# Kernel optimization log

Measured on AMD Instinct MI355X. Metric: run time of the kernel, lower is better.

Reference implementation:

```python
import jax, jax.numpy as jnp
from jax import lax
import numpy as np

B, DIM, HEADS, L, K = 8, 128, 8, 4096, 3
INNER = DIM * HEADS
PAD = K // 2
EPS = 1e-5
SCALE = DIM ** -0.5


def setup_inputs() -> dict:
    key = jax.random.key(0)
    ks = jax.random.split(key, 32)

    def n(i, shape, s):
        return jax.random.normal(ks[i], shape, jnp.float32) * s

    inp = {"x": jax.random.normal(ks[0], (B, DIM, L), jnp.float32)}
    inp["ln1_g"] = jnp.ones((DIM,), jnp.float32)
    inp["ln1_b"] = jnp.zeros((DIM,), jnp.float32)
    for idx, p in enumerate(("q", "k", "v")):
        base = 1 + idx * 2
        inp[p + "_dw"] = n(base, (DIM, 1, K), 0.2)        # depthwise kernel
        inp[p + "_bn_g"] = jnp.ones((DIM,), jnp.float32)
        inp[p + "_bn_b"] = jnp.zeros((DIM,), jnp.float32)
        inp[p + "_bn_m"] = jnp.zeros((DIM,), jnp.float32)  # running mean
        inp[p + "_bn_v"] = jnp.ones((DIM,), jnp.float32)   # running var
        inp[p + "_pw"] = n(base + 1, (INNER, DIM), 0.05)   # 1x1 conv dim->inner
    inp["dwc_dw"] = n(8, (DIM,), 0.2)                      # kernel-1 depthwise = per-channel scale
    inp["dwc_bn_g"] = jnp.ones((DIM,), jnp.float32)
    inp["dwc_bn_b"] = jnp.zeros((DIM,), jnp.float32)
    inp["dwc_bn_m"] = jnp.zeros((DIM,), jnp.float32)
    inp["dwc_bn_v"] = jnp.ones((DIM,), jnp.float32)
    inp["dwc_pw"] = n(9, (DIM, DIM), 0.05)
    inp["out_w"] = n(10, (DIM, INNER), 0.05)
    inp["out_b"] = jnp.zeros((DIM,), jnp.float32)
    inp["ln2_g"] = jnp.ones((DIM,), jnp.float32)
    inp["ln2_b"] = jnp.zeros((DIM,), jnp.float32)
    inp["ff_w1"] = n(11, (4 * DIM, DIM), 0.05)
    inp["ff_b1"] = jnp.zeros((4 * DIM,), jnp.float32)
    inp["ff_w2"] = n(12, (DIM, 4 * DIM), 0.05)
    inp["ff_b2"] = jnp.zeros((DIM,), jnp.float32)
    return inp


def _layernorm(x, g, b):
    # channel-wise LN over axis=1 (unbiased=False variance)
    m = jnp.mean(x, axis=1, keepdims=True)
    v = jnp.var(x, axis=1, keepdims=True)
    return (x - m) / jnp.sqrt(v + EPS) * g[None, :, None] + b[None, :, None]


def _dw_block(x, dw, g, b, m, v, pw):
    # depthwise conv (k=K, same padding) -> eval-mode BN -> 1x1 conv
    y = lax.conv_general_dilated(x, dw, (1,), [(PAD, PAD)],
                                 feature_group_count=DIM,
                                 dimension_numbers=("NCH", "OIH", "NCH"))
    y = (y - m[None, :, None]) * (g / jnp.sqrt(v + EPS))[None, :, None] + b[None, :, None]
    return jnp.einsum("oi,bil->bol", pw, y)


def reference(x, ln1_g, ln1_b,
              q_dw, q_bn_g, q_bn_b, q_bn_m, q_bn_v, q_pw,
              k_dw, k_bn_g, k_bn_b, k_bn_m, k_bn_v, k_pw,
              v_dw, v_bn_g, v_bn_b, v_bn_m, v_bn_v, v_pw,
              dwc_dw, dwc_bn_g, dwc_bn_b, dwc_bn_m, dwc_bn_v, dwc_pw,
              out_w, out_b, ln2_g, ln2_b, ff_w1, ff_b1, ff_w2, ff_b2):
    # ---- attention block (PreNorm + residual) ----
    xn = _layernorm(x, ln1_g, ln1_b)
    q = _dw_block(xn, q_dw, q_bn_g, q_bn_b, q_bn_m, q_bn_v, q_pw)  # [B, INNER, L]
    k = _dw_block(xn, k_dw, k_bn_g, k_bn_b, k_bn_m, k_bn_v, k_pw)
    v = _dw_block(xn, v_dw, v_bn_g, v_bn_b, v_bn_m, v_bn_v, v_pw)

    def split(t):  # b (h d) x -> (b h) x d
        return t.reshape(B, HEADS, DIM, L).transpose(0, 1, 3, 2).reshape(B * HEADS, L, DIM)

    q, k, v = split(q), split(k), split(v)
    k_soft = jax.nn.softmax(k, axis=-1)                       # softmax over feature dim d
    kk = jnp.einsum("nxd,nxe->nde", q, k_soft) * SCALE        # [(bh), d, d]
    # DWConv gate on q (kernel-1 depthwise -> BN -> 1x1), channels = DIM
    g_ = q * dwc_dw[None, None, :]
    g_ = (g_ - dwc_bn_m) * (dwc_bn_g / jnp.sqrt(dwc_bn_v + EPS)) + dwc_bn_b
    g_ = jnp.einsum("od,nxd->nxo", dwc_pw, g_)
    gate = jax.nn.sigmoid(g_) * v
    out = jnp.einsum("nxd,nde->nxe", v, kk) + gate            # [(bh), L, d]
    out = out.reshape(B, HEADS, L, DIM).transpose(0, 1, 3, 2).reshape(B, INNER, L)
    attn = jnp.einsum("oi,bil->bol", out_w, out) + out_b[None, :, None]
    x = attn + x

    # ---- feed-forward block (PreNorm + residual) ----
    xn = _layernorm(x, ln2_g, ln2_b)
    h = jnp.einsum("oi,bil->bol", ff_w1, xn) + ff_b1[None, :, None]
    h = jax.nn.gelu(h, approximate=False)
    h = jnp.einsum("oi,bil->bol", ff_w2, h) + ff_b2[None, :, None]
    return h + x
```

## Files before the change

### kernel.cpp

```cpp
#include <hip/hip_runtime.h>
#include <hip/hip_bf16.h>
#include <math.h>

#define DI __device__ __forceinline__

namespace {

constexpr int L = 4096;
constexpr float EPS = 1e-5f;
constexpr float SCALEF = 0.08838834764831845f;

typedef unsigned short u16;
typedef unsigned int u32;
typedef unsigned char u8;
typedef __attribute__((ext_vector_type(8))) short bf16x8;
typedef __attribute__((ext_vector_type(4))) float f32x4;

DI float b2f(u16 h){ u32 u = ((u32)h) << 16; float f; __builtin_memcpy(&f, &u, 4); return f; }
DI u16 f2b(float f){ u32 u; __builtin_memcpy(&u, &f, 4); u32 r = u + 0x7fffu + ((u >> 16) & 1u); return (u16)(r >> 16); }
DI float sigmoidf(float x){ return 1.f / (1.f + __expf(-x)); }

DI uint2 pack_fp8x8(const float* v){
  u32 lo = __builtin_amdgcn_cvt_pk_fp8_f32(v[0], v[1], 0, false);
  lo = (u32)__builtin_amdgcn_cvt_pk_fp8_f32(v[2], v[3], lo, true);
  u32 hi = __builtin_amdgcn_cvt_pk_fp8_f32(v[4], v[5], 0, false);
  hi = (u32)__builtin_amdgcn_cvt_pk_fp8_f32(v[6], v[7], hi, true);
  return make_uint2(lo, hi);
}
DI u8 f2e(float v){ return (u8)__builtin_amdgcn_cvt_pk_fp8_f32(v, v, 0, false); }
DI float e2f(u8 c){ return __builtin_amdgcn_cvt_f32_fp8((int)c, 0); }

DI int boff(int o, int d8){ return ((o >> 4) << 11) + (d8 << 7) + (((o & 15) ^ d8) << 3); }
DI int toff(int dhi, int nl, int x8){ return (dhi << 11) + (x8 << 7) + (((nl ^ x8 ^ dhi) & 15) << 3); }
DI int foff(int g, int k8, int nn){ return (g << 11) + (k8 << 7) + (nn << 3); }
DI int faddr(int x, int e){ return ((x >> 4) << 11) + ((e >> 3) << 7) + ((x & 15) << 3) + (e & 7); }

DI void stage_a(const u16* __restrict__ g, int rs, u16* a_s, int tid){
  #pragma unroll
  for (int it = 0; it < 4; it++){
    int item = tid + 256 * it;
    int d8 = item & 15, l = item >> 4;
    *(uint4*)&a_s[l * 136 + d8 * 8] = *(const uint4*)&g[(size_t)l * rs + d8 * 8];
  }
}

__global__ __launch_bounds__(256) void ln_kernel(
    const float* __restrict__ x, const float* __restrict__ g,
    const float* __restrict__ bt, u16* __restrict__ o)
{
  const int tid = threadIdx.x;
  const int pos = blockIdx.x * 64 + (tid >> 2);
  const int part = tid & 3;
  const int b = pos >> 12, l = pos & (L - 1);
  const float* xb = x + (size_t)b * 128 * L + l;
  float vv[32];
  float s = 0.f, ss = 0.f;
  #pragma unroll
  for (int i = 0; i < 32; i++){
    float v = xb[(size_t)(part * 32 + i) * L];
    vv[i] = v; s += v; ss += v * v;
  }
  s += __shfl_xor(s, 1);  s += __shfl_xor(s, 2);
  ss += __shfl_xor(ss, 1); ss += __shfl_xor(ss, 2);
  const float m = s * (1.f / 128.f);
  const float rs = rsqrtf(ss * (1.f / 128.f) - m * m + EPS);
  #pragma unroll
  for (int c = 0; c < 4; c++){
    u16 pk[8];
    #pragma unroll
    for (int j = 0; j < 8; j++){
      int d = part * 32 + c * 8 + j;
      pk[j] = f2b((vv[c * 8 + j] - m) * rs * g[d] + bt[d]);
    }
    uint4 uu; __builtin_memcpy(&uu, pk, 16);
    *(uint4*)&o[(size_t)pos * 128 + part * 32 + c * 8] = uu;
  }
}

__global__ __launch_bounds__(256) void wpack_kernel(
    const float* __restrict__ q_pw, const float* __restrict__ k_pw,
    const float* __restrict__ v_pw, const float* __restrict__ out_w,
    const float* __restrict__ ff_w1, const float* __restrict__ ff_w2,
    const float* __restrict__ dwc_dw, const float* __restrict__ dwc_bng,
    const float* __restrict__ dwc_bnb, const float* __restrict__ dwc_bnm,
    const float* __restrict__ dwc_bnv, const float* __restrict__ dwc_pw,
    u16* __restrict__ wpk, u16* __restrict__ w2tb, float* __restrict__ c2,
    u8* __restrict__ wpk8)
{
  const int blk = blockIdx.x;
  if (blk < 320){
    int item = blk * 256 + threadIdx.x;
    int d8 = item & 15;
    int o  = (item >> 4) & 127;
    int t  = item >> 11;
    const float* src;
    if (t < 24){
      int p = t >> 3, h = t & 7;
      const float* pw = (p == 0) ? q_pw : (p == 1 ? k_pw : v_pw);
      src = pw + (size_t)(h * 128 + o) * 128 + d8 * 8;
    } else if (t < 32){
      src = out_w + (size_t)o * 1024 + (t - 24) * 128 + d8 * 8;
    } else if (t < 36){
      src = ff_w1 + (size_t)((t - 32) * 128 + o) * 128 + d8 * 8;
    } else {
      src = ff_w2 + (size_t)o * 512 + (t - 36) * 128 + d8 * 8;
    }
    u16 pk[8];
    #pragma unroll
    for (int j = 0; j < 8; j++) pk[j] = f2b(src[j]);
    uint4 uu; __builtin_memcpy(&uu, pk, 16);
    *(uint4*)&wpk[(size_t)t * 16384 + boff(o, d8)] = uu;
  } else if (blk < 328){
    int item = (blk - 320) * 256 + threadIdx.x;
    int d8 = item & 15;
    int e  = item >> 4;
    u16 pk[8];
    #pragma unroll
    for (int j = 0; j < 8; j++){
      int d = d8 * 8 + j;
      float sD = dwc_bng[d] * rsqrtf(dwc_bnv[d] + EPS);
      pk[j] = f2b(dwc_pw[(size_t)e * 128 + d] * dwc_dw[d] * sD);
    }
    uint4 uu; __builtin_memcpy(&uu, pk, 16);
    *(uint4*)&w2tb[boff(e, d8)] = uu;
  } else if (blk == 328){
    int e = threadIdx.x;
    if (e < 128){
      float cacc = 0.f;
      for (int d = 0; d < 128; d++){
        float sD = dwc_bng[d] * rsqrtf(dwc_bnv[d] + EPS);
        cacc += dwc_pw[(size_t)e * 128 + d] * (dwc_bnb[d] - dwc_bnm[d] * sD);
      }
      c2[e] = cacc;
    }
  } else {
    int h = blk - 329;
    #pragma unroll
    for (int it = 0; it < 8; it++){
      int item = threadIdx.x + 256 * it;
      int nn = item & 15, k8 = (item >> 4) & 15, os = item >> 8;
      int o = os * 16 + nn;
      float fv[8];
      #pragma unroll
      for (int j = 0; j < 8; j++)
        fv[j] = out_w[(size_t)o * 1024 + h * 128 + k8 * 8 + j] * 16.f;
      *(uint2*)&wpk8[(h << 14) + foff(os, k8, nn)] = pack_fp8x8(fv);
    }
  }
}

struct QkvArgs {
  const float* dw[3];
  const float* bng[3];
  const float* bnb[3];
  const float* bnm[3];
  const float* bnv[3];
  void* outp[3];
};

__global__ __launch_bounds__(256, 3) void qkv_fused_kernel(
    const u16* __restrict__ xnb, const u16* __restrict__ wpk, QkvArgs args)
{
  __shared__ u16 y_s[64 * 136];
  __shared__ u16 w_s[128 * 128];
  __shared__ float4 coef[128];
  const int tid = threadIdx.x;
  const int lb = blockIdx.x;
  const int oh = blockIdx.y;
  const int bz = blockIdx.z;
  const int b  = bz / 3;
  const int p  = bz % 3;
  const int l0 = lb * 64;
  const int lane = tid & 63, wv = tid >> 6;
  const int nn = lane & 15, quad = lane >> 4;
  const int d8s = tid & 15;

  if (tid < 128){
    int d = tid;
    float sD = args.bng[p][d] * rsqrtf(args.bnv[p][d] + EPS);
    const float* dw = args.dw[p];
    coef[d] = make_float4(dw[d * 3] * sD, dw[d * 3 + 1] * sD, dw[d * 3 + 2] * sD,
                          args.bnb[p][d] - args.bnm[p][d] * sD);
  }
  __syncthreads();
  float4 cf[8];
  #pragma unroll
  for (int jj = 0; jj < 8; jj++) cf[jj] = coef[d8s * 8 + jj];
  #pragma unroll
  for (int it = 0; it < 4; it++){
    int l = (tid >> 4) + it * 16;
    int gl = l0 + l;
    const u16* rowp = xnb + ((size_t)b * L + gl) * 128 + d8s * 8;
    uint4 uc = *(const uint4*)rowp;
    uint4 um = (gl > 0)     ? *(const uint4*)(rowp - 128) : make_uint4(0, 0, 0, 0);
    uint4 up = (gl < L - 1) ? *(const uint4*)(rowp + 128) : make_uint4(0, 0, 0, 0);
    u16 em[8], ec[8], ep[8];
    __builtin_memcpy(em, &um, 16); __builtin_memcpy(ec, &uc, 16); __builtin_memcpy(ep, &up, 16);
    u16 pk[8];
    #pragma unroll
    for (int jj = 0; jj < 8; jj++)
      pk[jj] = f2b(cf[jj].x * b2f(em[jj]) + cf[jj].y * b2f(ec[jj]) + cf[jj].z * b2f(ep[jj]) + cf[jj].w);
    uint4 uu; __builtin_memcpy(&uu, pk, 16);
    *(uint4*)&y_s[l * 136 + d8s * 8] = uu;
  }
  __syncthreads();
  bf16x8 af[4];
  #pragma unroll
  for (int dc = 0; dc < 4; dc++)
    af[dc] = *(const bf16x8*)&y_s[(wv * 16 + nn) * 136 + ((dc << 2) + quad) * 8];

  for (int hh = 0; hh < 4; hh++){
    const int h = oh * 4 + hh;
    const int ph = p * 8 + h;
    if (hh) __syncthreads();
    const u16* src = wpk + ((size_t)ph << 14);
    #pragma unroll
    for (int it = 0; it < 8; it++){
      int idx = (tid + 256 * it) << 3;
      *(uint4*)&w_s[idx] = *(const uint4*)&src[idx];
    }
    __syncthreads();
    f32x4 acc[8];
    #pragma unroll
    for (int os = 0; os < 8; os++) acc[os] = (f32x4){0.f, 0.f, 0.f, 0.f};
    #pragma unroll
    for (int os = 0; os < 8; os++){
      #pragma unroll
      for (int dc = 0; dc < 4; dc++){
        int d8 = (dc << 2) + quad;
        bf16x8 bf = *(const bf16x8*)&w_s[(os << 11) + (d8 << 7) + ((nn ^ d8) << 3)];
        acc[os] = __builtin_amdgcn_mfma_f32_16x16x32_bf16(af[dc], bf, acc[os], 0, 0, 0);
      }
    }
    if (p == 1){
      #pragma unroll
      for (int r = 0; r < 4; r++){
        float m = acc[0][r];
        #pragma unroll
        for (int os = 1; os < 8; os++) m = fmaxf(m, acc[os][r]);
        m = fmaxf(m, __shfl_xor(m, 1));
        m = fmaxf(m, __shfl_xor(m, 2));
        m = fmaxf(m, __shfl_xor(m, 4));
        m = fmaxf(m, __shfl_xor(m, 8));
        float s = 0.f;
        #pragma unroll
        for (int os = 0; os < 8; os++){ acc[os][r] = __expf(acc[os][r] - m); s += acc[os][r]; }
        s += __shfl_xor(s, 1);
        s += __shfl_xor(s, 2);
        s += __shfl_xor(s, 4);
        s += __shfl_xor(s, 8);
        float inv = 1.f / s;
        #pragma unroll
        for (int os = 0; os < 8; os++) acc[os][r] *= inv;
      }
    }
    __syncthreads();
    u16* st = w_s;
    #pragma unroll
    for (int os = 0; os < 8; os++)
      #pragma unroll
      for (int r = 0; r < 4; r++)
        st[(wv * 16 + quad * 4 + r) * 136 + (os << 4) + nn] = f2b(acc[os][r]);
    __syncthreads();
    if (p == 2){
      u8* v8 = (u8*)args.outp[2];
      size_t tbase = ((size_t)((b * 8 + h) * 64 + lb)) << 13;
      #pragma unroll
      for (int it = 0; it < 4; it++){
        int g = it, e8 = tid >> 4, n2 = tid & 15;
        const u16* sp = &st[(g * 16 + n2) * 136 + e8 * 8];
        float fv[8];
        #pragma unroll
        for (int j = 0; j < 8; j++) fv[j] = b2f(sp[j]);
        *(uint2*)&v8[tbase + foff(g, e8, n2)] = pack_fp8x8(fv);
      }
    } else {
      u16* outp = (u16*)args.outp[p];
      size_t gbase = ((size_t)(b * 8 + h) * L + l0) * 128;
      #pragma unroll
      for (int it = 0; it < 4; it++){
        int row = (tid >> 4) + (it << 4);
        int c16 = tid & 15;
        *(uint4*)&outp[gbase + (size_t)row * 128 + (c16 << 3)] =
            *(const uint4*)&st[row * 136 + (c16 << 3)];
      }
    }
  }
}

__global__ __launch_bounds__(256, 2) void kk_kernel(
    const u16* __restrict__ qt, const u16* __restrict__ kt,
    float* __restrict__ kkp)
{
  __shared__ u16 qT[16384];
  __shared__ u16 kT[16384];
  const int tid = threadIdx.x;
  const int sp = blockIdx.x;
  const int n  = blockIdx.y;
  const int d8 = tid & 15;
  const int x8 = tid >> 4;
  const int lane = tid & 63, wv = tid >> 6;
  const int nn = lane & 15, quad = lane >> 4;
  const int m4 = (wv >> 1) << 2;
  const int e4 = (wv & 1) << 2;
  const size_t gbase = ((size_t)n * L + sp * 1024) * 128;

  uint4 rq[8], rk[8];
  #pragma unroll
  for (int j = 0; j < 8; j++){
    size_t off = gbase + (size_t)(x8 * 8 + j) * 128 + d8 * 8;
    rq[j] = *(const uint4*)&qt[off];
    rk[j] = *(const uint4*)&kt[off];
  }

  f32x4 acc[4][4];
  #pragma unroll
  for (int mi = 0; mi < 4; mi++)
    #pragma unroll
    for (int ei = 0; ei < 4; ei++) acc[mi][ei] = (f32x4){0.f, 0.f, 0.f, 0.f};

  for (int c = 0; c < 8; c++){
    #pragma unroll
    for (int i = 0; i < 8; i++){
      u16 cq[8], ck[8];
      #pragma unroll
      for (int j = 0; j < 8; j++){
        u16 tmp[8];
        __builtin_memcpy(tmp, &rq[j], 16); cq[j] = tmp[i];
        __builtin_memcpy(tmp, &rk[j], 16); ck[j] = tmp[i];
      }
      int off = toff(d8 >> 1, ((d8 & 1) << 3) + i, x8);
      uint4 uq, uk;
      __builtin_memcpy(&uq, cq, 16); __builtin_memcpy(&uk, ck, 16);
      *(uint4*)&qT[off] = uq;
      *(uint4*)&kT[off] = uk;
    }
    __syncthreads();
    if (c < 7){
      #pragma unroll
      for (int j = 0; j < 8; j++){
        size_t off = gbase + (size_t)((c + 1) * 128 + x8 * 8 + j) * 128 + d8 * 8;
        rq[j] = *(const uint4*)&qt[off];
        rk[j] = *(const uint4*)&kt[off];
      }
    }
    #pragma unroll
    for (int ks = 0; ks < 4; ks++){
      int x8f = (ks << 2) + quad;
      bf16x8 af[4], bf[4];
      #pragma unroll
      for (int t = 0; t < 4; t++){
        af[t] = *(const bf16x8*)&qT[toff(m4 + t, nn, x8f)];
        bf[t] = *(const bf16x8*)&kT[toff(e4 + t, nn, x8f)];
      }
      #pragma unroll
      for (int mi = 0; mi < 4; mi++)
        #pragma unroll
        for (int ei = 0; ei < 4; ei++)
          acc[mi][ei] = __builtin_amdgcn_mfma_f32_16x16x32_bf16(af[mi], bf[ei], acc[mi][ei], 0, 0, 0);
    }
    __syncthreads();
  }

  float* op = kkp + ((size_t)(sp * 64 + n) << 14);
  #pragma unroll
  for (int mi = 0; mi < 4; mi++){
    #pragma unroll
    for (int r = 0; r < 4; r++){
      int d = (m4 << 4) + mi * 16 + quad * 4 + r;
      #pragma unroll
      for (int ei = 0; ei < 4; ei++)
        op[d * 128 + (e4 << 4) + ei * 16 + nn] = acc[mi][ei][r];
    }
  }
}

__global__ __launch_bounds__(256) void kkred_kernel(
    const float* __restrict__ kkp, u8* __restrict__ kkbb8)
{
  int item = blockIdx.x * 256 + threadIdx.x;
  int nn = item & 15, d8 = (item >> 4) & 15, os = (item >> 8) & 7, n = item >> 11;
  int e = os * 16 + nn;
  float fv[8];
  #pragma unroll
  for (int j = 0; j < 8; j++){
    float s = 0.f;
    #pragma unroll
    for (int sp = 0; sp < 4; sp++)
      s += kkp[(size_t)sp * (64 * 16384) + n * 16384 + (d8 * 8 + j) * 128 + e];
    fv[j] = s * (SCALEF * 32.f);
  }
  *(uint2*)&kkbb8[((size_t)n << 14) + foff(os, d8, nn)] = pack_fp8x8(fv);
}

__global__ __launch_bounds__(256, 4) void gateout_kernel(
    const u16* __restrict__ qt, const u8* __restrict__ vt8,
    const u8* __restrict__ kkbb8, const u16* __restrict__ w2tb,
    const float* __restrict__ c2, u8* __restrict__ outt8)
{
  __shared__ u16 q_s[64 * 136];
  __shared__ __attribute__((aligned(16))) u8 v_s8[8192];
  const int tid = threadIdx.x;
  const int lb = blockIdx.x;
  const int n  = blockIdx.y;
  const int l0 = lb * 64;
  const int lane = tid & 63, wv = tid >> 6;
  const int nn = lane & 15, quad = lane >> 4;
  const size_t vtile = ((size_t)(n * 64 + lb)) << 13;

  stage_a(qt + ((size_t)n * L + l0) * 128, 128, q_s, tid);
  #pragma unroll
  for (int it = 0; it < 2; it++){
    int idx = (tid + 256 * it) << 4;
    *(uint4*)&v_s8[idx] = *(const uint4*)&vt8[vtile + idx];
  }
  __syncthreads();

  bf16x8 af_q[4];
  long av[4];
  #pragma unroll
  for (int dc = 0; dc < 4; dc++){
    af_q[dc] = *(const bf16x8*)&q_s[(wv * 16 + nn) * 136 + ((dc << 2) + quad) * 8];
    av[dc] = *(const long*)&v_s8[foff(wv, (dc << 2) + quad, nn)];
  }
  const u8* kb8 = kkbb8 + ((size_t)n << 14);
  f32x4 acc_o[8], acc_g[8];
  #pragma unroll
  for (int os = 0; os < 8; os++){ acc_o[os] = (f32x4){0,0,0,0}; acc_g[os] = (f32x4){0,0,0,0}; }
  #pragma unroll
  for (int os = 0; os < 8; os++){
    #pragma unroll
    for (int dc = 0; dc < 4; dc++){
      int d8 = (dc << 2) + quad;
      long bkk = *(const long*)&kb8[foff(os, d8, nn)];
      bf16x8 bw  = *(const bf16x8*)&w2tb[(os << 11) + (d8 << 7) + ((nn ^ d8) << 3)];
      acc_o[os] = __builtin_amdgcn_mfma_f32_16x16x32_fp8_fp8(av[dc], bkk, acc_o[os], 0, 0, 0);
      acc_g[os] = __builtin_amdgcn_mfma_f32_16x16x32_bf16(af_q[dc], bw, acc_g[os], 0, 0, 0);
    }
  }
  __syncthreads();
  u8* st8 = (u8*)q_s;
  #pragma unroll
  for (int os = 0; os < 8; os++){
    int e = (os << 4) + nn;
    float c2v = c2[e];
    #pragma unroll
    for (int r = 0; r < 4; r++){
      int xr = wv * 16 + quad * 4 + r;
      float ve = e2f(v_s8[faddr(xr, e)]);
      float val = acc_o[os][r] * (1.f / 32.f) + sigmoidf(acc_g[os][r] + c2v) * ve;
      st8[faddr(xr, e)] = f2e(val);
    }
  }
  __syncthreads();
  #pragma unroll
  for (int it = 0; it < 2; it++){
    int idx = (tid + 256 * it) << 4;
    *(uint4*)&outt8[vtile + idx] = *(const uint4*)&st8[idx];
  }
}

__global__ __launch_bounds__(256, 4) void outw_kernel(
    const u8* __restrict__ outt8, const u8* __restrict__ wpk8,
    const float* __restrict__ out_b, const float* __restrict__ x,
    const float* __restrict__ g2, const float* __restrict__ bt2,
    float* __restrict__ x2, u16* __restrict__ xn2b)
{
  __shared__ float stf[128 * 68];
  const int tid = threadIdx.x;
  const int lb = blockIdx.x;
  const int b  = blockIdx.y;
  const int l0 = lb * 64;
  const int lane = tid & 63, wv = tid >> 6;
  const int nn = lane & 15, quad = lane >> 4;
  f32x4 acc[8];
  #pragma unroll
  for (int os = 0; os < 8; os++) acc[os] = (f32x4){0,0,0,0};

  for (int h = 0; h < 8; h++){
    const size_t tbase = ((size_t)((b * 8 + h) * 64 + lb)) << 13;
    long af[4];
    #pragma unroll
    for (int dc = 0; dc < 4; dc++)
      af[dc] = *(const long*)&outt8[tbase + foff(wv, (dc << 2) + quad, nn)];
    const u8* bp8 = wpk8 + (h << 14);
    #pragma unroll
    for (int os = 0; os < 8; os++){
      #pragma unroll
      for (int dc = 0; dc < 4; dc++){
        long bf8 = *(const long*)&bp8[foff(os, (dc << 2) + quad, nn)];
        acc[os] = __builtin_amdgcn_mfma_f32_16x16x32_fp8_fp8(af[dc], bf8, acc[os], 0, 0, 0);
      }
    }
  }
  #pragma unroll
  for (int os = 0; os < 8; os++)
    #pragma unroll
    for (int r = 0; r < 4; r++)
      stf[((os << 4) + nn) * 68 + wv * 16 + quad * 4 + r] = acc[os][r] * 0.0625f;
  __syncthreads();
  {
    int o = tid >> 1, lh = tid & 1;
    float bias = out_b[o];
    size_t gbase = ((size_t)b * 128 + o) * L + l0 + lh * 32;
    float* sp = &stf[o * 68 + lh * 32];
    #pragma unroll
    for (int k = 0; k < 8; k++){
      float4 xv = *(const float4*)&x[gbase + k * 4];
      float4 sv = *(float4*)&sp[k * 4];
      float4 ov = make_float4(sv.x + bias + xv.x, sv.y + bias + xv.y,
                              sv.z + bias + xv.z, sv.w + bias + xv.w);
      *(float4*)&sp[k * 4] = ov;
      *(float4*)&x2[gbase + k * 4] = ov;
    }
  }
  __syncthreads();
  {
    int l = tid >> 2, part = tid & 3;
    float vv[32];
    float s = 0.f, ss = 0.f;
    #pragma unroll
    for (int i = 0; i < 32; i++){
      float v = stf[(part * 32 + i) * 68 + l];
      vv[i] = v; s += v; ss += v * v;
    }
    s += __shfl_xor(s, 1);  s += __shfl_xor(s, 2);
    ss += __shfl_xor(ss, 1); ss += __shfl_xor(ss, 2);
    float m = s * (1.f / 128.f);
    float rs = rsqrtf(ss * (1.f / 128.f) - m * m + EPS);
    #pragma unroll
    for (int c = 0; c < 4; c++){
      u16 pk[8];
      #pragma unroll
      for (int j = 0; j < 8; j++){
        int d = part * 32 + c * 8 + j;
        pk[j] = f2b((vv[c * 8 + j] - m) * rs * g2[d] + bt2[d]);
      }
      uint4 uu; __builtin_memcpy(&uu, pk, 16);
      *(uint4*)&xn2b[((size_t)b * L + l0 + l) * 128 + part * 32 + c * 8] = uu;
    }
  }
}

__global__ __launch_bounds__(256, 2) void ff_fused_kernel(
    const u16* __restrict__ xn2b, const u16* __restrict__ wpk,
    const float* __restrict__ b1, const float* __restrict__ b2,
    const float* __restrict__ x2, float* __restrict__ outp)
{
  __shared__ u16 a_s[64 * 136];
  __shared__ u16 h_s[64 * 136];
  const int tid = threadIdx.x;
  const int lb = blockIdx.x;
  const int b  = blockIdx.y;
  const int l0 = lb * 64;
  const int lane = tid & 63, wv = tid >> 6;
  const int nn = lane & 15, quad = lane >> 4;

  stage_a(xn2b + ((size_t)b * L + l0) * 128, 128, a_s, tid);
  __syncthreads();
  bf16x8 af[4];
  #pragma unroll
  for (int dc = 0; dc < 4; dc++)
    af[dc] = *(const bf16x8*)&a_s[(wv * 16 + nn) * 136 + ((dc << 2) + quad) * 8];

  f32x4 acc_out[8];
  #pragma unroll
  for (int os = 0; os < 8; os++) acc_out[os] = (f32x4){0.f, 0.f, 0.f, 0.f};

  for (int fc = 0; fc < 4; fc++){
    const u16* bp1 = wpk + (size_t)(32 + fc) * 16384;
    f32x4 hacc[8];
    #pragma unroll
    for (int os = 0; os < 8; os++) hacc[os] = (f32x4){0.f, 0.f, 0.f, 0.f};
    #pragma unroll
    for (int os = 0; os < 8; os++){
      #pragma unroll
      for (int dc = 0; dc < 4; dc++){
        int d8 = (dc << 2) + quad;
        bf16x8 bf = *(const bf16x8*)&bp1[(os << 11) + (d8 << 7) + ((nn ^ d8) << 3)];
        hacc[os] = __builtin_amdgcn_mfma_f32_16x16x32_bf16(af[dc], bf, hacc[os], 0, 0, 0);
      }
    }
    __syncthreads();
    #pragma unroll
    for (int os = 0; os < 8; os++){
      float bias = b1[fc * 128 + (os << 4) + nn];
      #pragma unroll
      for (int r = 0; r < 4; r++){
        float v = hacc[os][r] + bias;
        float ge = 0.5f * v * (1.f + erff(v * 0.70710678118654752f));
        h_s[(wv * 16 + quad * 4 + r) * 136 + (os << 4) + nn] = f2b(ge);
      }
    }
    __syncthreads();
    bf16x8 hf[4];
    #pragma unroll
    for (int dc = 0; dc < 4; dc++)
      hf[dc] = *(const bf16x8*)&h_s[(wv * 16 + nn) * 136 + ((dc << 2) + quad) * 8];
    const u16* bp2 = wpk + (size_t)(36 + fc) * 16384;
    #pragma unroll
    for (int os = 0; os < 8; os++){
      #pragma unroll
      for (int dc = 0; dc < 4; dc++){
        int d8 = (dc << 2) + quad;
        bf16x8 bf = *(const bf16x8*)&bp2[(os << 11) + (d8 << 7) + ((nn ^ d8) << 3)];
        acc_out[os] = __builtin_amdgcn_mfma_f32_16x16x32_bf16(hf[dc], bf, acc_out[os], 0, 0, 0);
      }
    }
  }

  float* stf = (float*)h_s;
  #pragma unroll
  for (int t = 0; t < 2; t++){
    __syncthreads();
    #pragma unroll
    for (int osl = 0; osl < 4; osl++){
      int os = t * 4 + osl;
      #pragma unroll
      for (int r = 0; r < 4; r++)
        stf[((osl << 4) + nn) * 68 + wv * 16 + quad * 4 + r] = acc_out[os][r];
    }
    __syncthreads();
    int ol = tid >> 2;
    int o  = t * 64 + ol;
    int lc = (tid & 3) * 16;
    float bias = b2[o];
    size_t gbase = ((size_t)b * 128 + o) * L + l0 + lc;
    #pragma unroll
    for (int k = 0; k < 4; k++){
      float4 sv = *(const float4*)&stf[ol * 68 + lc + k * 4];
      float4 xv = *(const float4*)&x2[gbase + k * 4];
      *(float4*)&outp[gbase + k * 4] = make_float4(sv.x + bias + xv.x, sv.y + bias + xv.y,
                                                   sv.z + bias + xv.z, sv.w + bias + xv.w);
    }
  }
}

}

extern "C" void kernel_launch(void* const* d_in, const int* in_sizes, int n_in,
                              void* d_out, int out_size, void* d_ws, size_t ws_size,
                              hipStream_t stream)
{
  const float* x      = (const float*)d_in[0];
  const float* ln1_g  = (const float*)d_in[1];
  const float* ln1_b  = (const float*)d_in[2];
  const float* q_dw   = (const float*)d_in[3];
  const float* q_bng  = (const float*)d_in[4];
  const float* q_bnb  = (const float*)d_in[5];
  const float* q_bnm  = (const float*)d_in[6];
  const float* q_bnv  = (const float*)d_in[7];
  const float* q_pw   = (const float*)d_in[8];
  const float* k_dw   = (const float*)d_in[9];
  const float* k_bng  = (const float*)d_in[10];
  const float* k_bnb  = (const float*)d_in[11];
  const float* k_bnm  = (const float*)d_in[12];
  const float* k_bnv  = (const float*)d_in[13];
  const float* k_pw   = (const float*)d_in[14];
  const float* v_dw   = (const float*)d_in[15];
  const float* v_bng  = (const float*)d_in[16];
  const float* v_bnb  = (const float*)d_in[17];
  const float* v_bnm  = (const float*)d_in[18];
  const float* v_bnv  = (const float*)d_in[19];
  const float* v_pw   = (const float*)d_in[20];
  const float* dwc_dw  = (const float*)d_in[21];
  const float* dwc_bng = (const float*)d_in[22];
  const float* dwc_bnb = (const float*)d_in[23];
  const float* dwc_bnm = (const float*)d_in[24];
  const float* dwc_bnv = (const float*)d_in[25];
  const float* dwc_pw  = (const float*)d_in[26];
  const float* out_w  = (const float*)d_in[27];
  const float* out_b  = (const float*)d_in[28];
  const float* ln2_g  = (const float*)d_in[29];
  const float* ln2_b  = (const float*)d_in[30];
  const float* ff_w1  = (const float*)d_in[31];
  const float* ff_b1  = (const float*)d_in[32];
  const float* ff_w2  = (const float*)d_in[33];
  const float* ff_b2  = (const float*)d_in[34];
  float* out = (float*)d_out;

  char* w = (char*)d_ws;
  u16*  qt    = (u16*)(w);
  u16*  kt    = (u16*)(w + (64ull  << 20));
  u8*   outt8 = (u8*)(w + (64ull  << 20));
  u8*   vt8   = (u8*)(w + (128ull << 20));
  u16*  xnb   = (u16*)(w + (192ull << 20));
  u8*   kkbb8 = (u8*)(w + (192ull << 20));
  u16*  xn2b  = (u16*)(w + (192ull << 20));
  float* kkp  = (float*)(w + (200ull << 20));
  float* x2   = kkp;
  u16*  w2tb  = (u16*)(w + (216ull << 20));
  float* c2   = (float*)(w + (216ull << 20) + 32768);
  u16*  wpk   = (u16*)(w + (216ull << 20) + 65536);
  u8*   wpk8  = (u8*)(w + (218ull << 20));

  ln_kernel<<<512, 256, 0, stream>>>(x, ln1_g, ln1_b, xnb);
  wpack_kernel<<<337, 256, 0, stream>>>(q_pw, k_pw, v_pw, out_w, ff_w1, ff_w2,
                                        dwc_dw, dwc_bng, dwc_bnb, dwc_bnm, dwc_bnv, dwc_pw,
                                        wpk, w2tb, c2, wpk8);

  QkvArgs qa;
  qa.dw[0] = q_dw;  qa.bng[0] = q_bng; qa.bnb[0] = q_bnb; qa.bnm[0] = q_bnm; qa.bnv[0] = q_bnv; qa.outp[0] = qt;
  qa.dw[1] = k_dw;  qa.bng[1] = k_bng; qa.bnb[1] = k_bnb; qa.bnm[1] = k_bnm; qa.bnv[1] = k_bnv; qa.outp[1] = kt;
  qa.dw[2] = v_dw;  qa.bng[2] = v_bng; qa.bnb[2] = v_bnb; qa.bnm[2] = v_bnm; qa.bnv[2] = v_bnv; qa.outp[2] = vt8;
  qkv_fused_kernel<<<dim3(64, 2, 24), 256, 0, stream>>>(xnb, wpk, qa);

  kk_kernel<<<dim3(4, 64), 256, 0, stream>>>(qt, kt, kkp);
  kkred_kernel<<<512, 256, 0, stream>>>(kkp, kkbb8);
  gateout_kernel<<<dim3(64, 64), 256, 0, stream>>>(qt, vt8, kkbb8, w2tb, c2, outt8);
  outw_kernel<<<dim3(64, 8), 256, 0, stream>>>(outt8, wpk8, out_b, x, ln2_g, ln2_b, x2, xn2b);

  ff_fused_kernel<<<dim3(64, 8), 256, 0, stream>>>(xn2b, wpk, ff_b1, ff_b2, x2, out);
}
```

Before: 378.3 us.

## Store q and k intermediates in fp8 and use fp8 MFMA for kk and gate

The q and softmaxed-k intermediates are now written as fp8, with k pre-scaled by 16 and the kk reduction scale adjusted to match. The kk kernel loads, transposes and multiplies fp8 tiles with fp8 MFMA, and the gate weights are packed as fp8 (scaled by 16, undone in the sigmoid argument) so gateout runs both products in fp8. This halves q/k memory traffic and LDS footprint and allows higher occupancy in kk_kernel, at the cost of reduced precision in the attention and gate paths.

```diff
diff --git a/kernel.cpp b/kernel.cpp
--- a/kernel.cpp
+++ b/kernel.cpp
@@ -31,9 +31,9 @@
 DI float e2f(u8 c){ return __builtin_amdgcn_cvt_f32_fp8((int)c, 0); }
 
 DI int boff(int o, int d8){ return ((o >> 4) << 11) + (d8 << 7) + (((o & 15) ^ d8) << 3); }
-DI int toff(int dhi, int nl, int x8){ return (dhi << 11) + (x8 << 7) + (((nl ^ x8 ^ dhi) & 15) << 3); }
 DI int foff(int g, int k8, int nn){ return (g << 11) + (k8 << 7) + (nn << 3); }
 DI int faddr(int x, int e){ return ((x >> 4) << 11) + ((e >> 3) << 7) + ((x & 15) << 3) + (e & 7); }
+DI int t8off(int dhi, int nl, int x8){ return (dhi << 11) + (x8 << 7) + (((nl ^ x8 ^ dhi) & 15) << 3); }
 
 DI void stage_a(const u16* __restrict__ g, int rs, u16* a_s, int tid){
   #pragma unroll
@@ -84,7 +84,7 @@
     const float* __restrict__ dwc_dw, const float* __restrict__ dwc_bng,
     const float* __restrict__ dwc_bnb, const float* __restrict__ dwc_bnm,
     const float* __restrict__ dwc_bnv, const float* __restrict__ dwc_pw,
-    u16* __restrict__ wpk, u16* __restrict__ w2tb, float* __restrict__ c2,
+    u16* __restrict__ wpk, u8* __restrict__ w2tb8, float* __restrict__ c2,
     u8* __restrict__ wpk8)
 {
   const int blk = blockIdx.x;
@@ -110,20 +110,22 @@
     for (int j = 0; j < 8; j++) pk[j] = f2b(src[j]);
     uint4 uu; __builtin_memcpy(&uu, pk, 16);
     *(uint4*)&wpk[(size_t)t * 16384 + boff(o, d8)] = uu;
-  } else if (blk < 328){
-    int item = (blk - 320) * 256 + threadIdx.x;
-    int d8 = item & 15;
-    int e  = item >> 4;
-    u16 pk[8];
-    #pragma unroll
-    for (int j = 0; j < 8; j++){
-      int d = d8 * 8 + j;
-      float sD = dwc_bng[d] * rsqrtf(dwc_bnv[d] + EPS);
-      pk[j] = f2b(dwc_pw[(size_t)e * 128 + d] * dwc_dw[d] * sD);
-    }
-    uint4 uu; __builtin_memcpy(&uu, pk, 16);
-    *(uint4*)&w2tb[boff(e, d8)] = uu;
-  } else if (blk == 328){
+  } else if (blk == 320){
+    #pragma unroll
+    for (int it = 0; it < 8; it++){
+      int item = threadIdx.x + 256 * it;
+      int nn = item & 15, k8 = (item >> 4) & 15, os = item >> 8;
+      int e = os * 16 + nn;
+      float fv[8];
+      #pragma unroll
+      for (int j = 0; j < 8; j++){
+        int d = k8 * 8 + j;
+        float sD = dwc_bng[d] * rsqrtf(dwc_bnv[d] + EPS);
+        fv[j] = dwc_pw[(size_t)e * 128 + d] * dwc_dw[d] * sD * 16.f;
+      }
+      *(uint2*)&w2tb8[foff(os, k8, nn)] = pack_fp8x8(fv);
+    }
+  } else if (blk == 321){
     int e = threadIdx.x;
     if (e < 128){
       float cacc = 0.f;
@@ -134,7 +136,7 @@
       c2[e] = cacc;
     }
   } else {
-    int h = blk - 329;
+    int h = blk - 322;
     #pragma unroll
     for (int it = 0; it < 8; it++){
       int item = threadIdx.x + 256 * it;
@@ -155,7 +157,7 @@
   const float* bnb[3];
   const float* bnm[3];
   const float* bnv[3];
-  void* outp[3];
+  u8* outp[3];
 };
 
 __global__ __launch_bounds__(256, 3) void qkv_fused_kernel(
@@ -249,7 +251,7 @@
         s += __shfl_xor(s, 2);
         s += __shfl_xor(s, 4);
         s += __shfl_xor(s, 8);
-        float inv = 1.f / s;
+        float inv = 16.f / s;
         #pragma unroll
         for (int os = 0; os < 8; os++) acc[os][r] *= inv;
       }
@@ -263,7 +265,7 @@
         st[(wv * 16 + quad * 4 + r) * 136 + (os << 4) + nn] = f2b(acc[os][r]);
     __syncthreads();
     if (p == 2){
-      u8* v8 = (u8*)args.outp[2];
+      u8* v8 = args.outp[2];
       size_t tbase = ((size_t)((b * 8 + h) * 64 + lb)) << 13;
       #pragma unroll
       for (int it = 0; it < 4; it++){
@@ -275,25 +277,28 @@
         *(uint2*)&v8[tbase + foff(g, e8, n2)] = pack_fp8x8(fv);
       }
     } else {
-      u16* outp = (u16*)args.outp[p];
+      u8* outp8 = args.outp[p];
       size_t gbase = ((size_t)(b * 8 + h) * L + l0) * 128;
       #pragma unroll
       for (int it = 0; it < 4; it++){
-        int row = (tid >> 4) + (it << 4);
-        int c16 = tid & 15;
-        *(uint4*)&outp[gbase + (size_t)row * 128 + (c16 << 3)] =
-            *(const uint4*)&st[row * 136 + (c16 << 3)];
-      }
-    }
-  }
-}
-
-__global__ __launch_bounds__(256, 2) void kk_kernel(
-    const u16* __restrict__ qt, const u16* __restrict__ kt,
+        int item = tid + 256 * it;
+        int row = item >> 4, d8 = item & 15;
+        const u16* sp = &st[row * 136 + d8 * 8];
+        float fv[8];
+        #pragma unroll
+        for (int j = 0; j < 8; j++) fv[j] = b2f(sp[j]);
+        *(uint2*)&outp8[gbase + (size_t)row * 128 + d8 * 8] = pack_fp8x8(fv);
+      }
+    }
+  }
+}
+
+__global__ __launch_bounds__(256, 3) void kk_kernel(
+    const u8* __restrict__ qt8, const u8* __restrict__ kt8,
     float* __restrict__ kkp)
 {
-  __shared__ u16 qT[16384];
-  __shared__ u16 kT[16384];
+  __shared__ u8 qT8[16384];
+  __shared__ u8 kT8[16384];
   const int tid = threadIdx.x;
   const int sp = blockIdx.x;
   const int n  = blockIdx.y;
@@ -305,12 +310,12 @@
   const int e4 = (wv & 1) << 2;
   const size_t gbase = ((size_t)n * L + sp * 1024) * 128;
 
-  uint4 rq[8], rk[8];
+  uint2 rq[8], rk[8];
   #pragma unroll
   for (int j = 0; j < 8; j++){
     size_t off = gbase + (size_t)(x8 * 8 + j) * 128 + d8 * 8;
-    rq[j] = *(const uint4*)&qt[off];
-    rk[j] = *(const uint4*)&kt[off];
+    rq[j] = *(const uint2*)&qt8[off];
+    rk[j] = *(const uint2*)&kt8[off];
   }
 
   f32x4 acc[4][4];
@@ -322,42 +327,43 @@
   for (int c = 0; c < 8; c++){
     #pragma unroll
     for (int i = 0; i < 8; i++){
-      u16 cq[8], ck[8];
+      u8 cq[8], ck[8];
       #pragma unroll
       for (int j = 0; j < 8; j++){
-        u16 tmp[8];
-        __builtin_memcpy(tmp, &rq[j], 16); cq[j] = tmp[i];
-        __builtin_memcpy(tmp, &rk[j], 16); ck[j] = tmp[i];
-      }
-      int off = toff(d8 >> 1, ((d8 & 1) << 3) + i, x8);
-      uint4 uq, uk;
-      __builtin_memcpy(&uq, cq, 16); __builtin_memcpy(&uk, ck, 16);
-      *(uint4*)&qT[off] = uq;
-      *(uint4*)&kT[off] = uk;
+        u8 tmp[8];
+        __builtin_memcpy(tmp, &rq[j], 8); cq[j] = tmp[i];
+        __builtin_memcpy(tmp, &rk[j], 8); ck[j] = tmp[i];
+      }
+      int d = d8 * 8 + i;
+      int off = t8off(d >> 4, d & 15, x8);
+      uint2 uq, uk;
+      __builtin_memcpy(&uq, cq, 8); __builtin_memcpy(&uk, ck, 8);
+      *(uint2*)&qT8[off] = uq;
+      *(uint2*)&kT8[off] = uk;
     }
     __syncthreads();
     if (c < 7){
       #pragma unroll
       for (int j = 0; j < 8; j++){
         size_t off = gbase + (size_t)((c + 1) * 128 + x8 * 8 + j) * 128 + d8 * 8;
-        rq[j] = *(const uint4*)&qt[off];
-        rk[j] = *(const uint4*)&kt[off];
+        rq[j] = *(const uint2*)&qt8[off];
+        rk[j] = *(const uint2*)&kt8[off];
       }
     }
     #pragma unroll
     for (int ks = 0; ks < 4; ks++){
       int x8f = (ks << 2) + quad;
-      bf16x8 af[4], bf[4];
+      long af[4], bf[4];
       #pragma unroll
       for (int t = 0; t < 4; t++){
-        af[t] = *(const bf16x8*)&qT[toff(m4 + t, nn, x8f)];
-        bf[t] = *(const bf16x8*)&kT[toff(e4 + t, nn, x8f)];
+        af[t] = *(const long*)&qT8[t8off(m4 + t, nn, x8f)];
+        bf[t] = *(const long*)&kT8[t8off(e4 + t, nn, x8f)];
       }
       #pragma unroll
       for (int mi = 0; mi < 4; mi++)
         #pragma unroll
         for (int ei = 0; ei < 4; ei++)
-          acc[mi][ei] = __builtin_amdgcn_mfma_f32_16x16x32_bf16(af[mi], bf[ei], acc[mi][ei], 0, 0, 0);
+          acc[mi][ei] = __builtin_amdgcn_mfma_f32_16x16x32_fp8_fp8(af[mi], bf[ei], acc[mi][ei], 0, 0, 0);
     }
     __syncthreads();
   }
@@ -388,17 +394,17 @@
     #pragma unroll
     for (int sp = 0; sp < 4; sp++)
       s += kkp[(size_t)sp * (64 * 16384) + n * 16384 + (d8 * 8 + j) * 128 + e];
-    fv[j] = s * (SCALEF * 32.f);
+    fv[j] = s * (SCALEF * 2.f);
   }
   *(uint2*)&kkbb8[((size_t)n << 14) + foff(os, d8, nn)] = pack_fp8x8(fv);
 }
 
 __global__ __launch_bounds__(256, 4) void gateout_kernel(
-    const u16* __restrict__ qt, const u8* __restrict__ vt8,
-    const u8* __restrict__ kkbb8, const u16* __restrict__ w2tb,
+    const u8* __restrict__ qt8, const u8* __restrict__ vt8,
+    const u8* __restrict__ kkbb8, const u8* __restrict__ w2tb8,
     const float* __restrict__ c2, u8* __restrict__ outt8)
 {
-  __shared__ u16 q_s[64 * 136];
+  __shared__ __attribute__((aligned(16))) u8 q_s8[64 * 144];
   __shared__ __attribute__((aligned(16))) u8 v_s8[8192];
   const int tid = threadIdx.x;
   const int lb = blockIdx.x;
@@ -407,8 +413,14 @@
   const int lane = tid & 63, wv = tid >> 6;
   const int nn = lane & 15, quad = lane >> 4;
   const size_t vtile = ((size_t)(n * 64 + lb)) << 13;
-
-  stage_a(qt + ((size_t)n * L + l0) * 128, 128, q_s, tid);
+  const size_t qbase = ((size_t)n * L + l0) * 128;
+
+  #pragma unroll
+  for (int it = 0; it < 4; it++){
+    int item = tid + 256 * it;
+    int d8b = item & 15, l = item >> 4;
+    *(uint2*)&q_s8[l * 144 + d8b * 8] = *(const uint2*)&qt8[qbase + (size_t)l * 128 + d8b * 8];
+  }
   #pragma unroll
   for (int it = 0; it < 2; it++){
     int idx = (tid + 256 * it) << 4;
@@ -416,11 +428,10 @@
   }
   __syncthreads();
 
-  bf16x8 af_q[4];
-  long av[4];
+  long aq[4], av[4];
   #pragma unroll
   for (int dc = 0; dc < 4; dc++){
-    af_q[dc] = *(const bf16x8*)&q_s[(wv * 16 + nn) * 136 + ((dc << 2) + quad) * 8];
+    aq[dc] = *(const long*)&q_s8[(wv * 16 + nn) * 144 + ((dc << 2) + quad) * 8];
     av[dc] = *(const long*)&v_s8[foff(wv, (dc << 2) + quad, nn)];
   }
   const u8* kb8 = kkbb8 + ((size_t)n << 14);
@@ -433,13 +444,13 @@
     for (int dc = 0; dc < 4; dc++){
       int d8 = (dc << 2) + quad;
       long bkk = *(const long*)&kb8[foff(os, d8, nn)];
-      bf16x8 bw  = *(const bf16x8*)&w2tb[(os << 11) + (d8 << 7) + ((nn ^ d8) << 3)];
+      long bw8 = *(const long*)&w2tb8[foff(os, d8, nn)];
       acc_o[os] = __builtin_amdgcn_mfma_f32_16x16x32_fp8_fp8(av[dc], bkk, acc_o[os], 0, 0, 0);
-      acc_g[os] = __builtin_amdgcn_mfma_f32_16x16x32_bf16(af_q[dc], bw, acc_g[os], 0, 0, 0);
+      acc_g[os] = __builtin_amdgcn_mfma_f32_16x16x32_fp8_fp8(aq[dc], bw8, acc_g[os], 0, 0, 0);
     }
   }
   __syncthreads();
-  u8* st8 = (u8*)q_s;
+  u8* st8 = q_s8;
   #pragma unroll
   for (int os = 0; os < 8; os++){
     int e = (os << 4) + nn;
@@ -448,7 +459,7 @@
     for (int r = 0; r < 4; r++){
       int xr = wv * 16 + quad * 4 + r;
       float ve = e2f(v_s8[faddr(xr, e)]);
-      float val = acc_o[os][r] * (1.f / 32.f) + sigmoidf(acc_g[os][r] + c2v) * ve;
+      float val = acc_o[os][r] * (1.f / 32.f) + sigmoidf(acc_g[os][r] * 0.0625f + c2v) * ve;
       st8[faddr(xr, e)] = f2e(val);
     }
   }
@@ -680,8 +691,8 @@
   float* out = (float*)d_out;
 
   char* w = (char*)d_ws;
-  u16*  qt    = (u16*)(w);
-  u16*  kt    = (u16*)(w + (64ull  << 20));
+  u8*   qt8   = (u8*)(w);
+  u8*   kt8   = (u8*)(w + (32ull  << 20));
   u8*   outt8 = (u8*)(w + (64ull  << 20));
   u8*   vt8   = (u8*)(w + (128ull << 20));
   u16*  xnb   = (u16*)(w + (192ull << 20));
@@ -689,25 +700,25 @@
   u16*  xn2b  = (u16*)(w + (192ull << 20));
   float* kkp  = (float*)(w + (200ull << 20));
   float* x2   = kkp;
-  u16*  w2tb  = (u16*)(w + (216ull << 20));
-  float* c2   = (float*)(w + (216ull << 20) + 32768);
+  u8*   w2tb8 = (u8*)(w + (216ull << 20));
+  float* c2   = (float*)(w + (216ull << 20) + 16384);
   u16*  wpk   = (u16*)(w + (216ull << 20) + 65536);
   u8*   wpk8  = (u8*)(w + (218ull << 20));
 
   ln_kernel<<<512, 256, 0, stream>>>(x, ln1_g, ln1_b, xnb);
-  wpack_kernel<<<337, 256, 0, stream>>>(q_pw, k_pw, v_pw, out_w, ff_w1, ff_w2,
+  wpack_kernel<<<330, 256, 0, stream>>>(q_pw, k_pw, v_pw, out_w, ff_w1, ff_w2,
                                         dwc_dw, dwc_bng, dwc_bnb, dwc_bnm, dwc_bnv, dwc_pw,
-                                        wpk, w2tb, c2, wpk8);
+                                        wpk, w2tb8, c2, wpk8);
 
   QkvArgs qa;
-  qa.dw[0] = q_dw;  qa.bng[0] = q_bng; qa.bnb[0] = q_bnb; qa.bnm[0] = q_bnm; qa.bnv[0] = q_bnv; qa.outp[0] = qt;
-  qa.dw[1] = k_dw;  qa.bng[1] = k_bng; qa.bnb[1] = k_bnb; qa.bnm[1] = k_bnm; qa.bnv[1] = k_bnv; qa.outp[1] = kt;
+  qa.dw[0] = q_dw;  qa.bng[0] = q_bng; qa.bnb[0] = q_bnb; qa.bnm[0] = q_bnm; qa.bnv[0] = q_bnv; qa.outp[0] = qt8;
+  qa.dw[1] = k_dw;  qa.bng[1] = k_bng; qa.bnb[1] = k_bnb; qa.bnm[1] = k_bnm; qa.bnv[1] = k_bnv; qa.outp[1] = kt8;
   qa.dw[2] = v_dw;  qa.bng[2] = v_bng; qa.bnb[2] = v_bnb; qa.bnm[2] = v_bnm; qa.bnv[2] = v_bnv; qa.outp[2] = vt8;
   qkv_fused_kernel<<<dim3(64, 2, 24), 256, 0, stream>>>(xnb, wpk, qa);
 
-  kk_kernel<<<dim3(4, 64), 256, 0, stream>>>(qt, kt, kkp);
+  kk_kernel<<<dim3(4, 64), 256, 0, stream>>>(qt8, kt8, kkp);
   kkred_kernel<<<512, 256, 0, stream>>>(kkp, kkbb8);
-  gateout_kernel<<<dim3(64, 64), 256, 0, stream>>>(qt, vt8, kkbb8, w2tb, c2, outt8);
+  gateout_kernel<<<dim3(64, 64), 256, 0, stream>>>(qt8, vt8, kkbb8, w2tb8, c2, outt8);
   outw_kernel<<<dim3(64, 8), 256, 0, stream>>>(outt8, wpk8, out_b, x, ln2_g, ln2_b, x2, xn2b);
 
   ff_fused_kernel<<<dim3(64, 8), 256, 0, stream>>>(xn2b, wpk, ff_b1, ff_b2, x2, out);
```

Result: no change. 383.3 us (+1.3%).
